# Kernel tuning notes

Measured on AMD Instinct MI355X. Metric: run time of the kernel, lower is better.

## Reference

```python
import jax, jax.numpy as jnp
import numpy as np

DIM = 2048
NH = 16
HD = DIM // NH  # 128


def setup_inputs() -> dict:
    key = jax.random.key(0)
    ks = jax.random.split(key, 9)
    s_in = 1.0 / np.sqrt(DIM)
    inp = {
        "x": jax.random.normal(ks[0], (2, 2048, DIM), dtype=jnp.float32),
        # torch Linear weights stored as (out, in); we keep (in, out) for x @ W
        "wq": jax.random.uniform(ks[1], (DIM, DIM), jnp.float32, -s_in, s_in),
        "bq": jax.random.uniform(ks[2], (DIM,), jnp.float32, -s_in, s_in),
        "wk": jax.random.uniform(ks[3], (DIM, HD), jnp.float32, -s_in, s_in),
        "bk": jax.random.uniform(ks[4], (HD,), jnp.float32, -s_in, s_in),
        "wv": jax.random.uniform(ks[5], (DIM, HD), jnp.float32, -s_in, s_in),
        "bv": jax.random.uniform(ks[6], (HD,), jnp.float32, -s_in, s_in),
        "wo": jax.random.uniform(ks[7], (DIM, DIM), jnp.float32, -s_in, s_in),
        "bo": jax.random.uniform(ks[8], (DIM,), jnp.float32, -s_in, s_in),
    }
    return inp


def reference(x, wq, bq, wk, bk, wv, bv, wo, bo):
    bs, sl, dim = x.shape
    q = x @ wq + bq                      # [b, s, dim]
    k = x @ wk + bk                      # [b, s, hd] (single shared KV head)
    v = x @ wv + bv                      # [b, s, hd]
    q = q.reshape(bs, sl, NH, HD)        # [b, s, h, hd]
    scale = 1.0 / np.sqrt(HD).astype(np.float32)
    # scores: broadcast single KV head over all query heads
    attn = jnp.einsum('bshd,btd->bhst', q, k) * scale   # [b, h, s, s]
    att = jax.nn.softmax(attn, axis=-1)
    o = jnp.einsum('bhst,btd->bshd', att, v)            # [b, s, h, hd]
    o = o.reshape(bs, sl, dim)
    return o @ wo + bo
```

## Files before the change

### kernel.cpp

```cpp
#include <hip/hip_runtime.h>
#include <hip/hip_bf16.h>
#include <math.h>

#define DIM 2048
#define NH 16
#define HD 128
#define BATCH 2
#define SEQ 2048
#define TOKENS (BATCH * SEQ)
#define NQKV (DIM + 2 * HD)

typedef __attribute__((ext_vector_type(8))) _Float16 f16x8;
typedef __attribute__((ext_vector_type(2))) _Float16 f16x2;
typedef __attribute__((ext_vector_type(4))) float f32x4;
typedef unsigned short u16;
typedef unsigned int u32;

typedef union { u32 d[4]; f16x8 v; } frag_u;

__device__ __forceinline__ u16 f2h(float f) {
    union { _Float16 h; u16 u; } v; v.h = (_Float16)f; return v.u;
}
__device__ __forceinline__ void gll16(const void* g, void* l) {
    __builtin_amdgcn_global_load_lds(
        (const __attribute__((address_space(1))) unsigned int*)g,
        (__attribute__((address_space(3))) unsigned int*)l, 16, 0, 0);
}

#define KIDX(r, c) ((r) * 128 + (((((c) << 1)) ^ (((r) & 7) << 4)) >> 1))
#define VIDX(d, c) ((d) * 64  + (((((c) << 1)) ^ (((d) & 7) << 4)) >> 1))

__global__ __launch_bounds__(256) void conv_f16(
    const float* __restrict__ in, u16* __restrict__ out)
{
    const int i = blockIdx.x * 256 + threadIdx.x;
    const float4 v = ((const float4*)in)[i];
    ushort4 h;
    h.x = f2h(v.x); h.y = f2h(v.y); h.z = f2h(v.z); h.w = f2h(v.w);
    ((ushort4*)out)[i] = h;
}

__global__ __launch_bounds__(256) void transpose_f16(
    const float* __restrict__ W, u16* __restrict__ T, int K, int N, int rowoff)
{
    __shared__ float tile[32][33];
    const int k0 = blockIdx.x * 32;
    const int n0 = blockIdx.y * 32;
    const int tid = threadIdx.x;
#pragma unroll
    for (int i = 0; i < 4; ++i) {
        const int idx = tid + i * 256;
        const int r = idx >> 5, c = idx & 31;
        tile[r][c] = W[(size_t)(k0 + r) * N + n0 + c];
    }
    __syncthreads();
#pragma unroll
    for (int i = 0; i < 4; ++i) {
        const int idx = tid + i * 256;
        const int r = idx >> 5, c = idx & 31;
        T[(size_t)(rowoff + n0 + r) * K + k0 + c] = f2h(tile[c][r]);
    }
}

__global__ __launch_bounds__(256) void concat_bias(
    const float* __restrict__ bq, const float* __restrict__ bk,
    const float* __restrict__ bv, float* __restrict__ bc)
{
    const int i = blockIdx.x * 256 + threadIdx.x;
    float v;
    if (i < DIM) v = bq[i];
    else if (i < DIM + HD) v = bk[i - DIM];
    else v = bv[i - DIM - HD];
    bc[i] = v;
}

template <int MODE>
__global__ __launch_bounds__(256) void gemm_f16(
    const u16* __restrict__ A, const u16* __restrict__ B,
    const float* __restrict__ bias, float* __restrict__ Cf,
    u16* __restrict__ qdst, u16* __restrict__ kdst, u16* __restrict__ vtdst,
    float scale)
{
    constexpr int BK = 32;
    __shared__ u16 lds[2][2 * 128 * BK];

    const int tid = threadIdx.x;
    const int wid = tid >> 6;
    const int lane = tid & 63;
    const int lr = lane & 15;
    const int lhi = lane >> 4;
    const int wr = wid >> 1, wc = wid & 1;
    const int bm = blockIdx.y * 128;
    const int bn = blockIdx.x * 128;

    f32x4 acc[4][4];
#pragma unroll
    for (int i = 0; i < 4; ++i)
#pragma unroll
        for (int j = 0; j < 4; ++j) acc[i][j] = (f32x4){0.f, 0.f, 0.f, 0.f};

#define STAGE(buf_, k0_)                                                      \
    {                                                                         \
        _Pragma("unroll")                                                     \
        for (int rr = 0; rr < 2; ++rr) {                                      \
            const int slot = rr * 256 + tid;                                  \
            const int row = slot >> 2;                                        \
            const int gch = ((slot & 3) ^ ((row >> 1) & 3)) * 8;              \
            char* lbase = (char*)lds[buf_] + (size_t)(rr * 256 + wid * 64) * 16; \
            gll16(A + (size_t)(bm + row) * DIM + (k0_) + gch, lbase);         \
            gll16(B + (size_t)(bn + row) * DIM + (k0_) + gch, lbase + 8192);  \
        }                                                                     \
    }

    STAGE(0, 0);
    __syncthreads();

    int cur = 0;
    for (int k0 = 0; k0 < DIM; k0 += BK) {
        if (k0 + BK < DIM) STAGE(cur ^ 1, k0 + BK);

        f16x8 a[4], b[4];
#pragma unroll
        for (int i = 0; i < 4; ++i) {
            const int mrow = wr * 64 + i * 16 + lr;
            const int nrow = wc * 64 + i * 16 + lr;
            a[i] = *(const f16x8*)&lds[cur][mrow * BK + ((lhi ^ ((mrow >> 1) & 3)) * 8)];
            b[i] = *(const f16x8*)&lds[cur][4096 + nrow * BK + ((lhi ^ ((nrow >> 1) & 3)) * 8)];
        }
        __builtin_amdgcn_s_setprio(1);
#pragma unroll
        for (int i = 0; i < 4; ++i)
#pragma unroll
            for (int j = 0; j < 4; ++j)
                acc[i][j] = __builtin_amdgcn_mfma_f32_16x16x32_f16(a[i], b[j], acc[i][j], 0, 0, 0);
        __builtin_amdgcn_s_setprio(0);
        __syncthreads();
        cur ^= 1;
    }
#undef STAGE

    const float alpha = (MODE == 0 && bn < DIM) ? scale : 1.0f;
    float bj[4];
#pragma unroll
    for (int j = 0; j < 4; ++j) bj[j] = bias[bn + wc * 64 + j * 16 + lr];

#pragma unroll
    for (int i = 0; i < 4; ++i) {
#pragma unroll
        for (int j = 0; j < 4; ++j) {
#pragma unroll
            for (int r = 0; r < 4; ++r) {
                const int row = bm + wr * 64 + i * 16 + lhi * 4 + r;
                const int col = bn + wc * 64 + j * 16 + lr;
                const float val = (acc[i][j][r] + bj[j]) * alpha;
                if (MODE == 1) {
                    Cf[(size_t)row * DIM + col] = val;
                } else if (bn < DIM) {
                    qdst[(size_t)row * DIM + col] = f2h(val);
                } else if (bn < DIM + HD) {
                    kdst[(size_t)row * HD + (col - DIM)] = f2h(val);
                } else {
                    vtdst[(size_t)(col - DIM - HD) * TOKENS + row] = f2h(val);
                }
            }
        }
    }
}

__global__ __launch_bounds__(256, 2) void mqa_attn_f16(
    const u16* __restrict__ Q, const u16* __restrict__ Kg,
    const u16* __restrict__ Vtg, u16* __restrict__ Oh)
{
    __shared__ __align__(16) u16 Ks[2][64 * 128];
    __shared__ __align__(16) u16 Vt[2][128 * 64];

    const int tid = threadIdx.x;
    const int wid = tid >> 6;
    const int lane = tid & 63;
    const int lr = lane & 15;
    const int lhi = lane >> 4;
    const bool l5 = (lhi & 2) != 0;

    const int qt = blockIdx.x;
    const int h  = blockIdx.y;
    const int b  = blockIdx.z;
    const size_t bseq = (size_t)b * SEQ;
    const int q0 = qt * 128 + wid * 32;

    f16x8 qf[2][4];
#pragma unroll
    for (int mt = 0; mt < 2; ++mt) {
        const u16* qrow = Q + (bseq + q0 + mt * 16 + lr) * DIM + (size_t)h * HD;
#pragma unroll
        for (int kk = 0; kk < 4; ++kk)
            qf[mt][kk] = *(const f16x8*)(qrow + kk * 32 + lhi * 8);
    }

    f16x8 ones;
#pragma unroll
    for (int j = 0; j < 8; ++j) ones[j] = (_Float16)1.0f;

    f32x4 o[2][8];
#pragma unroll
    for (int mt = 0; mt < 2; ++mt)
#pragma unroll
        for (int dt = 0; dt < 8; ++dt) o[mt][dt] = (f32x4){0.f, 0.f, 0.f, 0.f};
    float m[2]    = {-INFINITY, -INFINITY};
    float lsum[2] = {0.f, 0.f};

#define STAGE_KV(buf_, t0_)                                                   \
    {                                                                         \
        _Pragma("unroll")                                                     \
        for (int i = 0; i < 4; ++i) {                                         \
            const int L = i * 256 + tid;                                      \
            char* kbase = (char*)&Ks[buf_][0] + (size_t)(i * 256 + wid * 64) * 16; \
            char* vbase = (char*)&Vt[buf_][0] + (size_t)(i * 256 + wid * 64) * 16; \
            const int krow = L >> 4, kc = (L & 15) ^ ((L >> 4) & 7);          \
            const int vrow = L >> 3, vc = (L & 7) ^ ((L >> 3) & 7);           \
            gll16(&Kg[(bseq + (t0_) + krow) * HD + kc * 8], kbase);           \
            gll16(&Vtg[(size_t)vrow * TOKENS + bseq + (t0_) + vc * 8], vbase);\
        }                                                                     \
    }

    STAGE_KV(0, 0);
    __syncthreads();

    int cur = 0;
    for (int t0 = 0; t0 < SEQ; t0 += 64) {
        if (t0 + 64 < SEQ) STAGE_KV(cur ^ 1, t0 + 64);

        f32x4 sc[2][4];
#pragma unroll
        for (int mt = 0; mt < 2; ++mt)
#pragma unroll
            for (int ct = 0; ct < 4; ++ct) sc[mt][ct] = (f32x4){0.f, 0.f, 0.f, 0.f};
        __builtin_amdgcn_s_setprio(1);
#pragma unroll
        for (int kk = 0; kk < 4; ++kk)
#pragma unroll
            for (int ct = 0; ct < 4; ++ct) {
                const f16x8 kf = *(const f16x8*)&Ks[cur][KIDX(ct * 16 + lr, kk * 32 + lhi * 8)];
                sc[0][ct] = __builtin_amdgcn_mfma_f32_16x16x32_f16(kf, qf[0][kk], sc[0][ct], 0, 0, 0);
                sc[1][ct] = __builtin_amdgcn_mfma_f32_16x16x32_f16(kf, qf[1][kk], sc[1][ct], 0, 0, 0);
            }
        __builtin_amdgcn_s_setprio(0);

        frag_u pa[2][2];
        float al[2];
#pragma unroll
        for (int mt = 0; mt < 2; ++mt) {
            float pm = fmaxf(fmaxf(fmaxf(sc[mt][0][0], sc[mt][0][1]),
                                   fmaxf(sc[mt][0][2], sc[mt][0][3])),
                             fmaxf(fmaxf(sc[mt][1][0], sc[mt][1][1]),
                                   fmaxf(sc[mt][1][2], sc[mt][1][3])));
            pm = fmaxf(pm, fmaxf(fmaxf(fmaxf(sc[mt][2][0], sc[mt][2][1]),
                                       fmaxf(sc[mt][2][2], sc[mt][2][3])),
                                 fmaxf(fmaxf(sc[mt][3][0], sc[mt][3][1]),
                                       fmaxf(sc[mt][3][2], sc[mt][3][3]))));
            pm = fmaxf(pm, __shfl_xor(pm, 16));
            pm = fmaxf(pm, __shfl_xor(pm, 32));

            const bool grow = pm > m[mt] + 8.f;
            al[mt] = 1.f;
            if (__any(grow)) {
                if (grow) { al[mt] = __expf(m[mt] - pm); m[mt] = pm; }
#pragma unroll
                for (int dt = 0; dt < 8; ++dt)
#pragma unroll
                    for (int r = 0; r < 4; ++r)
                        o[mt][dt][r] *= al[mt];
            }

            u32 pk[4][2];
#pragma unroll
            for (int ct = 0; ct < 4; ++ct) {
                const float p0 = __expf(sc[mt][ct][0] - m[mt]);
                const float p1 = __expf(sc[mt][ct][1] - m[mt]);
                const float p2 = __expf(sc[mt][ct][2] - m[mt]);
                const float p3 = __expf(sc[mt][ct][3] - m[mt]);
                pk[ct][0] = __builtin_bit_cast(u32, __builtin_amdgcn_cvt_pkrtz(p0, p1));
                pk[ct][1] = __builtin_bit_cast(u32, __builtin_amdgcn_cvt_pkrtz(p2, p3));
            }

#pragma unroll
            for (int kk = 0; kk < 2; ++kk)
#pragma unroll
                for (int p = 0; p < 2; ++p) {
                    const u32 X = pk[2 * kk + 0][p];
                    const u32 Y = pk[2 * kk + 1][p];
                    const u32 sx = __shfl_xor(X, 32);
                    const u32 sy = __shfl_xor(Y, 32);
                    const u32 X1 = l5 ? sy : X;
                    const u32 Y1 = l5 ? Y : sx;
                    const auto u2 = __builtin_amdgcn_permlane16_swap(X1, Y1, false, false);
                    pa[mt][kk].d[p]     = u2[0];
                    pa[mt][kk].d[2 + p] = u2[1];
                }
        }

        f32x4 lacc[2];
        lacc[0] = (f32x4){0.f, 0.f, 0.f, 0.f};
        lacc[1] = (f32x4){0.f, 0.f, 0.f, 0.f};
        __builtin_amdgcn_s_setprio(1);
#pragma unroll
        for (int kk = 0; kk < 2; ++kk) {
            lacc[0] = __builtin_amdgcn_mfma_f32_16x16x32_f16(ones, pa[0][kk].v, lacc[0], 0, 0, 0);
            lacc[1] = __builtin_amdgcn_mfma_f32_16x16x32_f16(ones, pa[1][kk].v, lacc[1], 0, 0, 0);
#pragma unroll
            for (int dt = 0; dt < 8; ++dt) {
                const f16x8 vf = *(const f16x8*)&Vt[cur][VIDX(dt * 16 + lr, kk * 32 + lhi * 8)];
                o[0][dt] = __builtin_amdgcn_mfma_f32_16x16x32_f16(vf, pa[0][kk].v, o[0][dt], 0, 0, 0);
                o[1][dt] = __builtin_amdgcn_mfma_f32_16x16x32_f16(vf, pa[1][kk].v, o[1][dt], 0, 0, 0);
            }
        }
        __builtin_amdgcn_s_setprio(0);
#pragma unroll
        for (int mt = 0; mt < 2; ++mt)
            lsum[mt] = lsum[mt] * al[mt] + lacc[mt][0];

        __syncthreads();
        cur ^= 1;
    }
#undef STAGE_KV

#pragma unroll
    for (int mt = 0; mt < 2; ++mt) {
        const float inv = 1.f / lsum[mt];
        const size_t base = (bseq + q0 + mt * 16 + lr) * DIM + (size_t)h * HD + lhi * 4;
#pragma unroll
        for (int dt = 0; dt < 8; ++dt) {
            ushort4 h4;
            h4.x = f2h(o[mt][dt][0] * inv);
            h4.y = f2h(o[mt][dt][1] * inv);
            h4.z = f2h(o[mt][dt][2] * inv);
            h4.w = f2h(o[mt][dt][3] * inv);
            *(ushort4*)&Oh[base + dt * 16] = h4;
        }
    }
}

extern "C" void kernel_launch(void* const* d_in, const int* in_sizes, int n_in,
                              void* d_out, int out_size, void* d_ws, size_t ws_size,
                              hipStream_t stream) {
    const float* x  = (const float*)d_in[0];
    const float* wq = (const float*)d_in[1];
    const float* bq = (const float*)d_in[2];
    const float* wk = (const float*)d_in[3];
    const float* bk = (const float*)d_in[4];
    const float* wv = (const float*)d_in[5];
    const float* bv = (const float*)d_in[6];
    const float* wo = (const float*)d_in[7];
    const float* bo = (const float*)d_in[8];
    float* out = (float*)d_out;

    char* w = (char*)d_ws;
    u16* xh     = (u16*)w;                 w += (size_t)TOKENS * DIM * 2;
    u16* wcat   = (u16*)w;                 w += (size_t)NQKV * DIM * 2;
    u16* woT    = (u16*)w;                 w += (size_t)DIM * DIM * 2;
    u16* qb     = (u16*)w;                 w += (size_t)TOKENS * DIM * 2;
    u16* kb     = (u16*)w;                 w += (size_t)TOKENS * HD * 2;
    u16* vtb    = (u16*)w;                 w += (size_t)TOKENS * HD * 2;
    float* bc   = (float*)w;               w += 16384;
    u16* Oh = xh;

    const float scale = 0.08838834764831845f;
    const dim3 blk(256);

    conv_f16<<<TOKENS * DIM / 4 / 256, blk, 0, stream>>>(x, xh);
    transpose_f16<<<dim3(DIM / 32, DIM / 32), blk, 0, stream>>>(wq, wcat, DIM, DIM, 0);
    transpose_f16<<<dim3(DIM / 32, HD / 32), blk, 0, stream>>>(wk, wcat, DIM, HD, DIM);
    transpose_f16<<<dim3(DIM / 32, HD / 32), blk, 0, stream>>>(wv, wcat, DIM, HD, DIM + HD);
    transpose_f16<<<dim3(DIM / 32, DIM / 32), blk, 0, stream>>>(wo, woT, DIM, DIM, 0);
    concat_bias<<<NQKV / 256, blk, 0, stream>>>(bq, bk, bv, bc);

    gemm_f16<0><<<dim3(NQKV / 128, TOKENS / 128), blk, 0, stream>>>(
        xh, wcat, bc, nullptr, qb, kb, vtb, scale);

    mqa_attn_f16<<<dim3(SEQ / 128, NH, BATCH), blk, 0, stream>>>(qb, kb, vtb, Oh);

    gemm_f16<1><<<dim3(DIM / 128, TOKENS / 128), blk, 0, stream>>>(
        Oh, woT, bo, out, nullptr, nullptr, nullptr, 1.0f);
}
```

Before: 224.6 us.

## Triple-buffer GEMM LDS pipeline with single barrier and use exp2 softmax

The f16 GEMM moves from double to triple-buffered LDS staging. It prefetches two tiles ahead, waits with an explicit vmcnt, and uses one barrier per k-step instead of a trailing __syncthreads, so global loads overlap more with MFMA work. Separately, the attention softmax folds log2(e) into the Q scale and uses exp2f in place of __expf, with the rescale threshold adjusted to match. The triple buffer raises LDS use per block, which may lower occupancy.

New measurement: 252.2 us. 1.12x slower.

```diff
diff --git a/kernel.cpp b/kernel.cpp
--- a/kernel.cpp
+++ b/kernel.cpp
@@ -11,7 +11,6 @@
 #define NQKV (DIM + 2 * HD)
 
 typedef __attribute__((ext_vector_type(8))) _Float16 f16x8;
-typedef __attribute__((ext_vector_type(2))) _Float16 f16x2;
 typedef __attribute__((ext_vector_type(4))) float f32x4;
 typedef unsigned short u16;
 typedef unsigned int u32;
@@ -82,7 +81,9 @@
     float scale)
 {
     constexpr int BK = 32;
-    __shared__ u16 lds[2][2 * 128 * BK];
+    constexpr int NT = DIM / BK;
+    constexpr int BUFE = 2 * 128 * BK;
+    __shared__ u16 lds[3 * BUFE];
 
     const int tid = threadIdx.x;
     const int wid = tid >> 6;
@@ -99,33 +100,41 @@
 #pragma unroll
         for (int j = 0; j < 4; ++j) acc[i][j] = (f32x4){0.f, 0.f, 0.f, 0.f};
 
-#define STAGE(buf_, k0_)                                                      \
+#define STAGE(bp_, k0_)                                                       \
     {                                                                         \
         _Pragma("unroll")                                                     \
         for (int rr = 0; rr < 2; ++rr) {                                      \
             const int slot = rr * 256 + tid;                                  \
             const int row = slot >> 2;                                        \
             const int gch = ((slot & 3) ^ ((row >> 1) & 3)) * 8;              \
-            char* lbase = (char*)lds[buf_] + (size_t)(rr * 256 + wid * 64) * 16; \
+            char* lbase = (char*)(bp_) + (size_t)(rr * 256 + wid * 64) * 16;  \
             gll16(A + (size_t)(bm + row) * DIM + (k0_) + gch, lbase);         \
             gll16(B + (size_t)(bn + row) * DIM + (k0_) + gch, lbase + 8192);  \
         }                                                                     \
     }
 
-    STAGE(0, 0);
-    __syncthreads();
-
-    int cur = 0;
-    for (int k0 = 0; k0 < DIM; k0 += BK) {
-        if (k0 + BK < DIM) STAGE(cur ^ 1, k0 + BK);
+    STAGE(&lds[0], 0);
+    STAGE(&lds[BUFE], BK);
+
+    for (int t = 0; t < NT; ++t) {
+        if (t < NT - 1) {
+            asm volatile("s_waitcnt vmcnt(4)" ::: "memory");
+        } else {
+            asm volatile("s_waitcnt vmcnt(0)" ::: "memory");
+        }
+        __builtin_amdgcn_s_barrier();
+        asm volatile("" ::: "memory");
+
+        u16* buf = &lds[(t % 3) * BUFE];
+        if (t + 2 < NT) STAGE(&lds[((t + 2) % 3) * BUFE], (t + 2) * BK);
 
         f16x8 a[4], b[4];
 #pragma unroll
         for (int i = 0; i < 4; ++i) {
             const int mrow = wr * 64 + i * 16 + lr;
             const int nrow = wc * 64 + i * 16 + lr;
-            a[i] = *(const f16x8*)&lds[cur][mrow * BK + ((lhi ^ ((mrow >> 1) & 3)) * 8)];
-            b[i] = *(const f16x8*)&lds[cur][4096 + nrow * BK + ((lhi ^ ((nrow >> 1) & 3)) * 8)];
+            a[i] = *(const f16x8*)&buf[mrow * BK + ((lhi ^ ((mrow >> 1) & 3)) * 8)];
+            b[i] = *(const f16x8*)&buf[4096 + nrow * BK + ((lhi ^ ((nrow >> 1) & 3)) * 8)];
         }
         __builtin_amdgcn_s_setprio(1);
 #pragma unroll
@@ -134,8 +143,6 @@
             for (int j = 0; j < 4; ++j)
                 acc[i][j] = __builtin_amdgcn_mfma_f32_16x16x32_f16(a[i], b[j], acc[i][j], 0, 0, 0);
         __builtin_amdgcn_s_setprio(0);
-        __syncthreads();
-        cur ^= 1;
     }
 #undef STAGE
 
@@ -260,10 +267,10 @@
             pm = fmaxf(pm, __shfl_xor(pm, 16));
             pm = fmaxf(pm, __shfl_xor(pm, 32));
 
-            const bool grow = pm > m[mt] + 8.f;
+            const bool grow = pm > m[mt] + 11.5415604f;
             al[mt] = 1.f;
             if (__any(grow)) {
-                if (grow) { al[mt] = __expf(m[mt] - pm); m[mt] = pm; }
+                if (grow) { al[mt] = exp2f(m[mt] - pm); m[mt] = pm; }
 #pragma unroll
                 for (int dt = 0; dt < 8; ++dt)
 #pragma unroll
@@ -274,10 +281,10 @@
             u32 pk[4][2];
 #pragma unroll
             for (int ct = 0; ct < 4; ++ct) {
-                const float p0 = __expf(sc[mt][ct][0] - m[mt]);
-                const float p1 = __expf(sc[mt][ct][1] - m[mt]);
-                const float p2 = __expf(sc[mt][ct][2] - m[mt]);
-                const float p3 = __expf(sc[mt][ct][3] - m[mt]);
+                const float p0 = exp2f(sc[mt][ct][0] - m[mt]);
+                const float p1 = exp2f(sc[mt][ct][1] - m[mt]);
+                const float p2 = exp2f(sc[mt][ct][2] - m[mt]);
+                const float p3 = exp2f(sc[mt][ct][3] - m[mt]);
                 pk[ct][0] = __builtin_bit_cast(u32, __builtin_amdgcn_cvt_pkrtz(p0, p1));
                 pk[ct][1] = __builtin_bit_cast(u32, __builtin_amdgcn_cvt_pkrtz(p2, p3));
             }
@@ -363,7 +370,7 @@
     float* bc   = (float*)w;               w += 16384;
     u16* Oh = xh;
 
-    const float scale = 0.08838834764831845f;
+    const float scale = 0.08838834764831845f * 1.4426950408889634f;
     const dim3 blk(256);
 
     conv_f16<<<TOKENS * DIM / 4 / 256, blk, 0, stream>>>(x, xh);
```

## Software-pipeline attention: overlap previous tile's PV MFMA with current softmax

Applied to the files above, without the earlier changes.

Restructures the attention inner loop so the P·V matmul for the previous key tile runs right after the current QK^T scores, before the softmax exponentials. The goal is to let MFMA work overlap the VALU-heavy exp and shuffle work within each wave. V staging moves to a triple buffer so the previous tile stays resident, and the rescaling of o and lsum is deferred and applied after the delayed PV accumulation. This costs extra LDS (a third V buffer), more live registers for the pending P fragments, and an epilogue for the last tile.

Measured after the change: 223.1 us. About the same (-0.7%).

```diff
diff --git a/kernel.cpp b/kernel.cpp
--- a/kernel.cpp
+++ b/kernel.cpp
@@ -11,7 +11,6 @@
 #define NQKV (DIM + 2 * HD)
 
 typedef __attribute__((ext_vector_type(8))) _Float16 f16x8;
-typedef __attribute__((ext_vector_type(2))) _Float16 f16x2;
 typedef __attribute__((ext_vector_type(4))) float f32x4;
 typedef unsigned short u16;
 typedef unsigned int u32;
@@ -172,7 +171,7 @@
     const u16* __restrict__ Vtg, u16* __restrict__ Oh)
 {
     __shared__ __align__(16) u16 Ks[2][64 * 128];
-    __shared__ __align__(16) u16 Vt[2][128 * 64];
+    __shared__ __align__(16) u16 Vt[3][128 * 64];
 
     const int tid = threadIdx.x;
     const int wid = tid >> 6;
@@ -208,26 +207,47 @@
     float m[2]    = {-INFINITY, -INFINITY};
     float lsum[2] = {0.f, 0.f};
 
-#define STAGE_KV(buf_, t0_)                                                   \
+    frag_u pa[2][2];
+#pragma unroll
+    for (int mt = 0; mt < 2; ++mt)
+#pragma unroll
+        for (int kk = 0; kk < 2; ++kk)
+#pragma unroll
+            for (int p = 0; p < 4; ++p) pa[mt][kk].d[p] = 0u;
+
+#define STAGE_K(buf_, t0_)                                                    \
     {                                                                         \
         _Pragma("unroll")                                                     \
         for (int i = 0; i < 4; ++i) {                                         \
             const int L = i * 256 + tid;                                      \
             char* kbase = (char*)&Ks[buf_][0] + (size_t)(i * 256 + wid * 64) * 16; \
+            const int krow = L >> 4, kc = (L & 15) ^ ((L >> 4) & 7);          \
+            gll16(&Kg[(bseq + (t0_) + krow) * HD + kc * 8], kbase);           \
+        }                                                                     \
+    }
+#define STAGE_V(buf_, t0_)                                                    \
+    {                                                                         \
+        _Pragma("unroll")                                                     \
+        for (int i = 0; i < 4; ++i) {                                         \
+            const int L = i * 256 + tid;                                      \
             char* vbase = (char*)&Vt[buf_][0] + (size_t)(i * 256 + wid * 64) * 16; \
-            const int krow = L >> 4, kc = (L & 15) ^ ((L >> 4) & 7);          \
             const int vrow = L >> 3, vc = (L & 7) ^ ((L >> 3) & 7);           \
-            gll16(&Kg[(bseq + (t0_) + krow) * HD + kc * 8], kbase);           \
             gll16(&Vtg[(size_t)vrow * TOKENS + bseq + (t0_) + vc * 8], vbase);\
         }                                                                     \
     }
 
-    STAGE_KV(0, 0);
+    STAGE_K(0, 0);
+    STAGE_V(0, 0);
     __syncthreads();
 
-    int cur = 0;
+    int kcur = 0;
+    int vprev = 0, vcur = 0, vnxt = 1;
+
     for (int t0 = 0; t0 < SEQ; t0 += 64) {
-        if (t0 + 64 < SEQ) STAGE_KV(cur ^ 1, t0 + 64);
+        if (t0 + 64 < SEQ) {
+            STAGE_K(kcur ^ 1, t0 + 64);
+            STAGE_V(vnxt, t0 + 64);
+        }
 
         f32x4 sc[2][4];
 #pragma unroll
@@ -239,14 +259,32 @@
         for (int kk = 0; kk < 4; ++kk)
 #pragma unroll
             for (int ct = 0; ct < 4; ++ct) {
-                const f16x8 kf = *(const f16x8*)&Ks[cur][KIDX(ct * 16 + lr, kk * 32 + lhi * 8)];
+                const f16x8 kf = *(const f16x8*)&Ks[kcur][KIDX(ct * 16 + lr, kk * 32 + lhi * 8)];
                 sc[0][ct] = __builtin_amdgcn_mfma_f32_16x16x32_f16(kf, qf[0][kk], sc[0][ct], 0, 0, 0);
                 sc[1][ct] = __builtin_amdgcn_mfma_f32_16x16x32_f16(kf, qf[1][kk], sc[1][ct], 0, 0, 0);
             }
         __builtin_amdgcn_s_setprio(0);
 
-        frag_u pa[2][2];
-        float al[2];
+        f32x4 lacc[2];
+        lacc[0] = (f32x4){0.f, 0.f, 0.f, 0.f};
+        lacc[1] = (f32x4){0.f, 0.f, 0.f, 0.f};
+        __builtin_amdgcn_s_setprio(1);
+#pragma unroll
+        for (int kk = 0; kk < 2; ++kk) {
+            lacc[0] = __builtin_amdgcn_mfma_f32_16x16x32_f16(ones, pa[0][kk].v, lacc[0], 0, 0, 0);
+            lacc[1] = __builtin_amdgcn_mfma_f32_16x16x32_f16(ones, pa[1][kk].v, lacc[1], 0, 0, 0);
+#pragma unroll
+            for (int dt = 0; dt < 8; ++dt) {
+                const f16x8 vf = *(const f16x8*)&Vt[vprev][VIDX(dt * 16 + lr, kk * 32 + lhi * 8)];
+                o[0][dt] = __builtin_amdgcn_mfma_f32_16x16x32_f16(vf, pa[0][kk].v, o[0][dt], 0, 0, 0);
+                o[1][dt] = __builtin_amdgcn_mfma_f32_16x16x32_f16(vf, pa[1][kk].v, o[1][dt], 0, 0, 0);
+            }
+        }
+        __builtin_amdgcn_s_setprio(0);
+
+        frag_u panew[2][2];
+        float mnew[2];
+        bool grow[2];
 #pragma unroll
         for (int mt = 0; mt < 2; ++mt) {
             float pm = fmaxf(fmaxf(fmaxf(sc[mt][0][0], sc[mt][0][1]),
@@ -260,28 +298,19 @@
             pm = fmaxf(pm, __shfl_xor(pm, 16));
             pm = fmaxf(pm, __shfl_xor(pm, 32));
 
-            const bool grow = pm > m[mt] + 8.f;
-            al[mt] = 1.f;
-            if (__any(grow)) {
-                if (grow) { al[mt] = __expf(m[mt] - pm); m[mt] = pm; }
-#pragma unroll
-                for (int dt = 0; dt < 8; ++dt)
-#pragma unroll
-                    for (int r = 0; r < 4; ++r)
-                        o[mt][dt][r] *= al[mt];
-            }
+            grow[mt] = pm > m[mt] + 8.f;
+            mnew[mt] = grow[mt] ? pm : m[mt];
 
             u32 pk[4][2];
 #pragma unroll
             for (int ct = 0; ct < 4; ++ct) {
-                const float p0 = __expf(sc[mt][ct][0] - m[mt]);
-                const float p1 = __expf(sc[mt][ct][1] - m[mt]);
-                const float p2 = __expf(sc[mt][ct][2] - m[mt]);
-                const float p3 = __expf(sc[mt][ct][3] - m[mt]);
+                const float p0 = __expf(sc[mt][ct][0] - mnew[mt]);
+                const float p1 = __expf(sc[mt][ct][1] - mnew[mt]);
+                const float p2 = __expf(sc[mt][ct][2] - mnew[mt]);
+                const float p3 = __expf(sc[mt][ct][3] - mnew[mt]);
                 pk[ct][0] = __builtin_bit_cast(u32, __builtin_amdgcn_cvt_pkrtz(p0, p1));
                 pk[ct][1] = __builtin_bit_cast(u32, __builtin_amdgcn_cvt_pkrtz(p2, p3));
             }
-
 #pragma unroll
             for (int kk = 0; kk < 2; ++kk)
 #pragma unroll
@@ -293,35 +322,54 @@
                     const u32 X1 = l5 ? sy : X;
                     const u32 Y1 = l5 ? Y : sx;
                     const auto u2 = __builtin_amdgcn_permlane16_swap(X1, Y1, false, false);
-                    pa[mt][kk].d[p]     = u2[0];
-                    pa[mt][kk].d[2 + p] = u2[1];
+                    panew[mt][kk].d[p]     = u2[0];
+                    panew[mt][kk].d[2 + p] = u2[1];
                 }
         }
 
+#pragma unroll
+        for (int mt = 0; mt < 2; ++mt) {
+            lsum[mt] += lacc[mt][0];
+            if (__any(grow[mt])) {
+                const float al = grow[mt] ? __expf(m[mt] - mnew[mt]) : 1.f;
+#pragma unroll
+                for (int dt = 0; dt < 8; ++dt)
+#pragma unroll
+                    for (int r = 0; r < 4; ++r)
+                        o[mt][dt][r] *= al;
+                lsum[mt] *= al;
+            }
+            m[mt] = mnew[mt];
+#pragma unroll
+            for (int kk = 0; kk < 2; ++kk)
+                pa[mt][kk] = panew[mt][kk];
+        }
+
+        __syncthreads();
+        kcur ^= 1;
+        vprev = vcur; vcur = vnxt; vnxt = (vnxt + 1 == 3) ? 0 : vnxt + 1;
+    }
+#undef STAGE_K
+#undef STAGE_V
+
+    {
         f32x4 lacc[2];
         lacc[0] = (f32x4){0.f, 0.f, 0.f, 0.f};
         lacc[1] = (f32x4){0.f, 0.f, 0.f, 0.f};
-        __builtin_amdgcn_s_setprio(1);
 #pragma unroll
         for (int kk = 0; kk < 2; ++kk) {
             lacc[0] = __builtin_amdgcn_mfma_f32_16x16x32_f16(ones, pa[0][kk].v, lacc[0], 0, 0, 0);
             lacc[1] = __builtin_amdgcn_mfma_f32_16x16x32_f16(ones, pa[1][kk].v, lacc[1], 0, 0, 0);
 #pragma unroll
             for (int dt = 0; dt < 8; ++dt) {
-                const f16x8 vf = *(const f16x8*)&Vt[cur][VIDX(dt * 16 + lr, kk * 32 + lhi * 8)];
+                const f16x8 vf = *(const f16x8*)&Vt[vprev][VIDX(dt * 16 + lr, kk * 32 + lhi * 8)];
                 o[0][dt] = __builtin_amdgcn_mfma_f32_16x16x32_f16(vf, pa[0][kk].v, o[0][dt], 0, 0, 0);
                 o[1][dt] = __builtin_amdgcn_mfma_f32_16x16x32_f16(vf, pa[1][kk].v, o[1][dt], 0, 0, 0);
             }
         }
-        __builtin_amdgcn_s_setprio(0);
-#pragma unroll
-        for (int mt = 0; mt < 2; ++mt)
-            lsum[mt] = lsum[mt] * al[mt] + lacc[mt][0];
-
-        __syncthreads();
-        cur ^= 1;
-    }
-#undef STAGE_KV
+        lsum[0] += lacc[0][0];
+        lsum[1] += lacc[1][0];
+    }
 
 #pragma unroll
     for (int mt = 0; mt < 2; ++mt) {
```

## Split attention KV sequence across two wave groups with in-block merge

Applied to the files above, without the earlier changes.

The attention kernel now runs 512 threads per block: two groups of four waves each process half of the KV sequence (32-token tiles) for the same 128 queries, then merge their partial softmax state (max, sum, output) through shared memory before writing. This doubles waves per block to hide latency and shortens each wave's serial loop, at the cost of an extra merge step, smaller per-iteration MFMA batches, and higher register and LDS pressure under launch bounds of 4. The rescale is also moved after the P packing, and lsum rescaling is folded into the conditional branch.

Result: slower. 248.9 us (+10.8%).

```diff
diff --git a/kernel.cpp b/kernel.cpp
--- a/kernel.cpp
+++ b/kernel.cpp
@@ -11,7 +11,6 @@
 #define NQKV (DIM + 2 * HD)
 
 typedef __attribute__((ext_vector_type(8))) _Float16 f16x8;
-typedef __attribute__((ext_vector_type(2))) _Float16 f16x2;
 typedef __attribute__((ext_vector_type(4))) float f32x4;
 typedef unsigned short u16;
 typedef unsigned int u32;
@@ -26,9 +25,6 @@
         (const __attribute__((address_space(1))) unsigned int*)g,
         (__attribute__((address_space(3))) unsigned int*)l, 16, 0, 0);
 }
-
-#define KIDX(r, c) ((r) * 128 + (((((c) << 1)) ^ (((r) & 7) << 4)) >> 1))
-#define VIDX(d, c) ((d) * 64  + (((((c) << 1)) ^ (((d) & 7) << 4)) >> 1))
 
 __global__ __launch_bounds__(256) void conv_f16(
     const float* __restrict__ in, u16* __restrict__ out)
@@ -167,12 +163,11 @@
     }
 }
 
-__global__ __launch_bounds__(256, 2) void mqa_attn_f16(
+__global__ __launch_bounds__(512, 4) void mqa_attn_f16(
     const u16* __restrict__ Q, const u16* __restrict__ Kg,
     const u16* __restrict__ Vtg, u16* __restrict__ Oh)
 {
-    __shared__ __align__(16) u16 Ks[2][64 * 128];
-    __shared__ __align__(16) u16 Vt[2][128 * 64];
+    __shared__ __align__(16) u16 smem[32768];
 
     const int tid = threadIdx.x;
     const int wid = tid >> 6;
@@ -180,12 +175,20 @@
     const int lr = lane & 15;
     const int lhi = lane >> 4;
     const bool l5 = (lhi & 2) != 0;
+    const int qg = wid & 3;
+    const int half = wid >> 2;
 
     const int qt = blockIdx.x;
     const int h  = blockIdx.y;
     const int b  = blockIdx.z;
     const size_t bseq = (size_t)b * SEQ;
-    const int q0 = qt * 128 + wid * 32;
+    const int q0 = qt * 128 + qg * 32;
+    const int kvoff = half * 1024;
+
+#define KS(hh, bb, r, c) smem[((hh) * 2 + (bb)) * 4096 + (r) * 128 + \
+                              ((((c) >> 3) ^ ((r) & 7)) << 3)]
+#define VS(hh, bb, d, c) smem[16384 + ((hh) * 2 + (bb)) * 4096 + (d) * 32 + \
+                              (((((c) >> 3) & 3) ^ ((d) & 3)) << 3)]
 
     f16x8 qf[2][4];
 #pragma unroll
@@ -208,17 +211,20 @@
     float m[2]    = {-INFINITY, -INFINITY};
     float lsum[2] = {0.f, 0.f};
 
-#define STAGE_KV(buf_, t0_)                                                   \
+#define STAGE_KV(buf_, t_)                                                    \
     {                                                                         \
+        const int Ls = wid * 64 + lane;                                       \
+        const int krow = Ls >> 4;                                             \
+        const int kc = (Ls & 15) ^ (krow & 7);                                \
+        const int vrow = Ls >> 2;                                             \
+        const int vg = (Ls & 3) ^ (vrow & 3);                                 \
         _Pragma("unroll")                                                     \
-        for (int i = 0; i < 4; ++i) {                                         \
-            const int L = i * 256 + tid;                                      \
-            char* kbase = (char*)&Ks[buf_][0] + (size_t)(i * 256 + wid * 64) * 16; \
-            char* vbase = (char*)&Vt[buf_][0] + (size_t)(i * 256 + wid * 64) * 16; \
-            const int krow = L >> 4, kc = (L & 15) ^ ((L >> 4) & 7);          \
-            const int vrow = L >> 3, vc = (L & 7) ^ ((L >> 3) & 7);           \
-            gll16(&Kg[(bseq + (t0_) + krow) * HD + kc * 8], kbase);           \
-            gll16(&Vtg[(size_t)vrow * TOKENS + bseq + (t0_) + vc * 8], vbase);\
+        for (int i = 0; i < 2; ++i) {                                         \
+            char* kb = (char*)smem + (size_t)((i * 2 + (buf_)) * 4096 + wid * 512) * 2; \
+            char* vb = (char*)smem + (size_t)(16384 + (i * 2 + (buf_)) * 4096 + wid * 512) * 2; \
+            const int kv0 = i * 1024 + (t_) * 32;                             \
+            gll16(&Kg[(bseq + kv0 + krow) * HD + kc * 8], kb);                \
+            gll16(&Vtg[(size_t)vrow * TOKENS + bseq + kv0 + vg * 8], vb);     \
         }                                                                     \
     }
 
@@ -226,115 +232,134 @@
     __syncthreads();
 
     int cur = 0;
-    for (int t0 = 0; t0 < SEQ; t0 += 64) {
-        if (t0 + 64 < SEQ) STAGE_KV(cur ^ 1, t0 + 64);
-
-        f32x4 sc[2][4];
+    for (int t = 0; t < 32; ++t) {
+        if (t + 1 < 32) STAGE_KV(cur ^ 1, t + 1);
+
+        f32x4 sc[2][2];
 #pragma unroll
         for (int mt = 0; mt < 2; ++mt)
 #pragma unroll
-            for (int ct = 0; ct < 4; ++ct) sc[mt][ct] = (f32x4){0.f, 0.f, 0.f, 0.f};
+            for (int ct = 0; ct < 2; ++ct) sc[mt][ct] = (f32x4){0.f, 0.f, 0.f, 0.f};
         __builtin_amdgcn_s_setprio(1);
 #pragma unroll
         for (int kk = 0; kk < 4; ++kk)
 #pragma unroll
-            for (int ct = 0; ct < 4; ++ct) {
-                const f16x8 kf = *(const f16x8*)&Ks[cur][KIDX(ct * 16 + lr, kk * 32 + lhi * 8)];
+            for (int ct = 0; ct < 2; ++ct) {
+                const f16x8 kf = *(const f16x8*)&KS(half, cur, ct * 16 + lr, kk * 32 + lhi * 8);
                 sc[0][ct] = __builtin_amdgcn_mfma_f32_16x16x32_f16(kf, qf[0][kk], sc[0][ct], 0, 0, 0);
                 sc[1][ct] = __builtin_amdgcn_mfma_f32_16x16x32_f16(kf, qf[1][kk], sc[1][ct], 0, 0, 0);
             }
         __builtin_amdgcn_s_setprio(0);
 
-        frag_u pa[2][2];
+        frag_u pa[2];
         float al[2];
+        bool anyg[2];
 #pragma unroll
         for (int mt = 0; mt < 2; ++mt) {
             float pm = fmaxf(fmaxf(fmaxf(sc[mt][0][0], sc[mt][0][1]),
                                    fmaxf(sc[mt][0][2], sc[mt][0][3])),
                              fmaxf(fmaxf(sc[mt][1][0], sc[mt][1][1]),
                                    fmaxf(sc[mt][1][2], sc[mt][1][3])));
-            pm = fmaxf(pm, fmaxf(fmaxf(fmaxf(sc[mt][2][0], sc[mt][2][1]),
-                                       fmaxf(sc[mt][2][2], sc[mt][2][3])),
-                                 fmaxf(fmaxf(sc[mt][3][0], sc[mt][3][1]),
-                                       fmaxf(sc[mt][3][2], sc[mt][3][3]))));
             pm = fmaxf(pm, __shfl_xor(pm, 16));
             pm = fmaxf(pm, __shfl_xor(pm, 32));
 
             const bool grow = pm > m[mt] + 8.f;
-            al[mt] = 1.f;
-            if (__any(grow)) {
-                if (grow) { al[mt] = __expf(m[mt] - pm); m[mt] = pm; }
+            const float mnew = grow ? pm : m[mt];
+            al[mt] = grow ? __expf(m[mt] - mnew) : 1.f;
+            anyg[mt] = __any(grow);
+            m[mt] = mnew;
+
+            u32 pk[2][2];
+#pragma unroll
+            for (int ct = 0; ct < 2; ++ct) {
+                const float p0 = __expf(sc[mt][ct][0] - mnew);
+                const float p1 = __expf(sc[mt][ct][1] - mnew);
+                const float p2 = __expf(sc[mt][ct][2] - mnew);
+                const float p3 = __expf(sc[mt][ct][3] - mnew);
+                pk[ct][0] = __builtin_bit_cast(u32, __builtin_amdgcn_cvt_pkrtz(p0, p1));
+                pk[ct][1] = __builtin_bit_cast(u32, __builtin_amdgcn_cvt_pkrtz(p2, p3));
+            }
+#pragma unroll
+            for (int p = 0; p < 2; ++p) {
+                const u32 X = pk[0][p];
+                const u32 Y = pk[1][p];
+                const u32 sx = __shfl_xor(X, 32);
+                const u32 sy = __shfl_xor(Y, 32);
+                const u32 X1 = l5 ? sy : X;
+                const u32 Y1 = l5 ? Y : sx;
+                const auto u2 = __builtin_amdgcn_permlane16_swap(X1, Y1, false, false);
+                pa[mt].d[p]     = u2[0];
+                pa[mt].d[2 + p] = u2[1];
+            }
+
+            if (anyg[mt]) {
 #pragma unroll
                 for (int dt = 0; dt < 8; ++dt)
 #pragma unroll
                     for (int r = 0; r < 4; ++r)
                         o[mt][dt][r] *= al[mt];
-            }
-
-            u32 pk[4][2];
-#pragma unroll
-            for (int ct = 0; ct < 4; ++ct) {
-                const float p0 = __expf(sc[mt][ct][0] - m[mt]);
-                const float p1 = __expf(sc[mt][ct][1] - m[mt]);
-                const float p2 = __expf(sc[mt][ct][2] - m[mt]);
-                const float p3 = __expf(sc[mt][ct][3] - m[mt]);
-                pk[ct][0] = __builtin_bit_cast(u32, __builtin_amdgcn_cvt_pkrtz(p0, p1));
-                pk[ct][1] = __builtin_bit_cast(u32, __builtin_amdgcn_cvt_pkrtz(p2, p3));
-            }
-
-#pragma unroll
-            for (int kk = 0; kk < 2; ++kk)
-#pragma unroll
-                for (int p = 0; p < 2; ++p) {
-                    const u32 X = pk[2 * kk + 0][p];
-                    const u32 Y = pk[2 * kk + 1][p];
-                    const u32 sx = __shfl_xor(X, 32);
-                    const u32 sy = __shfl_xor(Y, 32);
-                    const u32 X1 = l5 ? sy : X;
-                    const u32 Y1 = l5 ? Y : sx;
-                    const auto u2 = __builtin_amdgcn_permlane16_swap(X1, Y1, false, false);
-                    pa[mt][kk].d[p]     = u2[0];
-                    pa[mt][kk].d[2 + p] = u2[1];
-                }
+                lsum[mt] *= al[mt];
+            }
         }
 
         f32x4 lacc[2];
         lacc[0] = (f32x4){0.f, 0.f, 0.f, 0.f};
         lacc[1] = (f32x4){0.f, 0.f, 0.f, 0.f};
         __builtin_amdgcn_s_setprio(1);
-#pragma unroll
-        for (int kk = 0; kk < 2; ++kk) {
-            lacc[0] = __builtin_amdgcn_mfma_f32_16x16x32_f16(ones, pa[0][kk].v, lacc[0], 0, 0, 0);
-            lacc[1] = __builtin_amdgcn_mfma_f32_16x16x32_f16(ones, pa[1][kk].v, lacc[1], 0, 0, 0);
-#pragma unroll
-            for (int dt = 0; dt < 8; ++dt) {
-                const f16x8 vf = *(const f16x8*)&Vt[cur][VIDX(dt * 16 + lr, kk * 32 + lhi * 8)];
-                o[0][dt] = __builtin_amdgcn_mfma_f32_16x16x32_f16(vf, pa[0][kk].v, o[0][dt], 0, 0, 0);
-                o[1][dt] = __builtin_amdgcn_mfma_f32_16x16x32_f16(vf, pa[1][kk].v, o[1][dt], 0, 0, 0);
-            }
+        lacc[0] = __builtin_amdgcn_mfma_f32_16x16x32_f16(ones, pa[0].v, lacc[0], 0, 0, 0);
+        lacc[1] = __builtin_amdgcn_mfma_f32_16x16x32_f16(ones, pa[1].v, lacc[1], 0, 0, 0);
+#pragma unroll
+        for (int dt = 0; dt < 8; ++dt) {
+            const f16x8 vf = *(const f16x8*)&VS(half, cur, dt * 16 + lr, lhi * 8);
+            o[0][dt] = __builtin_amdgcn_mfma_f32_16x16x32_f16(vf, pa[0].v, o[0][dt], 0, 0, 0);
+            o[1][dt] = __builtin_amdgcn_mfma_f32_16x16x32_f16(vf, pa[1].v, o[1][dt], 0, 0, 0);
         }
         __builtin_amdgcn_s_setprio(0);
-#pragma unroll
-        for (int mt = 0; mt < 2; ++mt)
-            lsum[mt] = lsum[mt] * al[mt] + lacc[mt][0];
+        lsum[0] += lacc[0][0];
+        lsum[1] += lacc[1][0];
 
         __syncthreads();
         cur ^= 1;
     }
 #undef STAGE_KV
-
+#undef KS
+#undef VS
+
+    float* fs = (float*)smem;
 #pragma unroll
     for (int mt = 0; mt < 2; ++mt) {
-        const float inv = 1.f / lsum[mt];
-        const size_t base = (bseq + q0 + mt * 16 + lr) * DIM + (size_t)h * HD + lhi * 4;
-#pragma unroll
-        for (int dt = 0; dt < 8; ++dt) {
-            ushort4 h4;
-            h4.x = f2h(o[mt][dt][0] * inv);
-            h4.y = f2h(o[mt][dt][1] * inv);
-            h4.z = f2h(o[mt][dt][2] * inv);
-            h4.w = f2h(o[mt][dt][3] * inv);
-            *(ushort4*)&Oh[base + dt * 16] = h4;
+        __syncthreads();
+        if (half == 1) {
+#pragma unroll
+            for (int dt = 0; dt < 8; ++dt)
+#pragma unroll
+                for (int r = 0; r < 4; ++r)
+                    fs[qg * 2048 + (dt * 4 + r) * 64 + lane] = o[mt][dt][r];
+            if (lhi == 0) {
+                fs[8192 + qg * 16 + lr] = m[mt];
+                fs[8192 + 64 + qg * 16 + lr] = lsum[mt];
+            }
+        }
+        __syncthreads();
+        if (half == 0) {
+            const float m1 = fs[8192 + qg * 16 + lr];
+            const float l1 = fs[8192 + 64 + qg * 16 + lr];
+            const float mm = fmaxf(m[mt], m1);
+            const float a0 = __expf(m[mt] - mm);
+            const float a1 = __expf(m1 - mm);
+            const float inv = 1.f / (lsum[mt] * a0 + l1 * a1);
+            const size_t base = (bseq + q0 + mt * 16 + lr) * DIM + (size_t)h * HD + lhi * 4;
+#pragma unroll
+            for (int dt = 0; dt < 8; ++dt) {
+                ushort4 h4;
+#pragma unroll
+                for (int r = 0; r < 4; ++r) {
+                    const float o1 = fs[qg * 2048 + (dt * 4 + r) * 64 + lane];
+                    const float val = (o[mt][dt][r] * a0 + o1 * a1) * inv;
+                    ((u16*)&h4)[r] = f2h(val);
+                }
+                *(ushort4*)&Oh[base + dt * 16] = h4;
+            }
         }
     }
 }
@@ -376,7 +401,7 @@
     gemm_f16<0><<<dim3(NQKV / 128, TOKENS / 128), blk, 0, stream>>>(
         xh, wcat, bc, nullptr, qb, kb, vtb, scale);
 
-    mqa_attn_f16<<<dim3(SEQ / 128, NH, BATCH), blk, 0, stream>>>(qb, kb, vtb, Oh);
+    mqa_attn_f16<<<dim3(SEQ / 128, NH, BATCH), dim3(512), 0, stream>>>(qb, kb, vtb, Oh);
 
     gemm_f16<1><<<dim3(DIM / 128, TOKENS / 128), blk, 0, stream>>>(
         Oh, woT, bo, out, nullptr, nullptr, nullptr, 1.0f);
```
